# Kernel tuning notes

Hardware: AMD Instinct MI355X
Metric: run time of the kernel (lower is better)

## Reference

```python
import jax, jax.numpy as jnp
import numpy as np

B, T, S, E, H = 2, 2048, 2048, 1024, 16
DH = E // H

def setup_inputs() -> dict:
    key = jax.random.key(0)
    ks = jax.random.split(key, 12)
    sc = 1.0 / np.sqrt(E)
    inp = {
        'query': jax.random.normal(ks[0], (B, T, E), jnp.float32),
        'key':   jax.random.normal(ks[1], (B, S, E), jnp.float32),
        'value': jax.random.normal(ks[2], (B, S, E), jnp.float32),
        'Wq': jax.random.normal(ks[3], (E, E), jnp.float32) * sc,
        'bq': jnp.zeros((E,), jnp.float32),
        'Wk': jax.random.normal(ks[4], (E, E), jnp.float32) * sc,
        'bk': jnp.zeros((E,), jnp.float32),
        'Wv': jax.random.normal(ks[5], (E, E), jnp.float32) * sc,
        'bv': jnp.zeros((E,), jnp.float32),
        'Wo': jax.random.normal(ks[6], (E, E), jnp.float32) * sc,
        'bo': jnp.zeros((E,), jnp.float32),
    }
    return inp

def reference(query, key, value, Wq, bq, Wk, bk, Wv, bv, Wo, bo):
    # Linear projections (torch nn.Linear: x @ W.T + b)
    Q = query @ Wq.T + bq          # [B,T,E]
    K = key   @ Wk.T + bk          # [B,S,E]
    V = value @ Wv.T + bv          # [B,S,E]
    # split heads -> [B,H,L,DH]
    Q = Q.reshape(B, T, H, DH).transpose(0, 2, 1, 3)
    K = K.reshape(B, S, H, DH).transpose(0, 2, 1, 3)
    V = V.reshape(B, S, H, DH).transpose(0, 2, 1, 3)
    scores = jnp.einsum('bhtd,bhsd->bhts', Q, K) / jnp.sqrt(jnp.float32(DH))
    attn = jax.nn.softmax(scores, axis=-1)            # [B,H,T,S]
    out = jnp.einsum('bhts,bhsd->bhtd', attn, V)      # [B,H,T,DH]
    out = out.transpose(0, 2, 1, 3).reshape(B, T, E)
    out = out @ Wo.T + bo                             # [B,T,E]
    attn_avg = attn.mean(axis=1)                      # average_attn_weights=True
    return out, attn_avg
```

## Files before the change

kernel.cpp:

```cpp
#include <hip/hip_runtime.h>

#define DEV __device__ __forceinline__

typedef __attribute__((ext_vector_type(8))) short short8;
typedef __attribute__((ext_vector_type(4))) float floatx4;
typedef __attribute__((ext_vector_type(2))) unsigned int uint2v;
typedef unsigned short u16;

DEV u16 f2bf(float f) {
  unsigned int u = __float_as_uint(f);
  u += 0x7fffu + ((u >> 16) & 1u);
  return (u16)(u >> 16);
}

DEV unsigned int pk2bf(float a, float b) {
  unsigned int ua = __float_as_uint(a) + 0x8000u;
  unsigned int ub = __float_as_uint(b) + 0x8000u;
  return (ua >> 16) | (ub & 0xffff0000u);
}

DEV void load16_to_lds(const void* g, void* l) {
  __builtin_amdgcn_global_load_lds(
      (const __attribute__((address_space(1))) unsigned int*)g,
      (__attribute__((address_space(3))) unsigned int*)l, 16, 0, 0);
}

#define MFMA16(A, B, C) __builtin_amdgcn_mfma_f32_16x16x32_bf16(A, B, C, 0, 0, 0)
#define EXP2(x) __builtin_amdgcn_exp2f(x)

#define QSCALE 0.18033688011112042f

DEV void stage_block(const u16* src_row0, int k0, int ln, void* ldsbase) {
  int r = ln >> 2;
  int p = ((ln & 3) - (ln >> 4)) & 3;
  load16_to_lds((const char*)(src_row0 + (size_t)r * 1024 + k0) + p * 16, ldsbase);
}
DEV const short8* frag_addr(const u16* base, int blk, int c, int q) {
  int slot = c * 4 + ((q + (c >> 2)) & 3);
  return (const short8*)(base + blk * 512 + slot * 8);
}

__global__ __launch_bounds__(256) void cvt_all(
    const float* __restrict__ w0, const float* __restrict__ w1,
    const float* __restrict__ w2, const float* __restrict__ w3,
    const float* __restrict__ a0, const float* __restrict__ a1, const float* __restrict__ a2,
    u16* __restrict__ e0, u16* __restrict__ e1, u16* __restrict__ e2, u16* __restrict__ e3,
    u16* __restrict__ f0, u16* __restrict__ f1, u16* __restrict__ f2) {
  const int t = blockIdx.y;
  const float* s;
  u16* d;
  size_t base;
  if (t < 4) {
    s = t == 0 ? w0 : t == 1 ? w1 : t == 2 ? w2 : w3;
    d = t == 0 ? e0 : t == 1 ? e1 : t == 2 ? e2 : e3;
    base = 0;
  } else {
    int a = (t - 4) >> 2;
    s = a == 0 ? a0 : a == 1 ? a1 : a2;
    d = a == 0 ? f0 : a == 1 ? f1 : f2;
    base = (size_t)((t - 4) & 3) * 1048576;
  }
  size_t i = base + (size_t)(blockIdx.x * 256 + threadIdx.x) * 4;
  float4 v = *(const float4*)(s + i);
  ushort4 o;
  o.x = f2bf(v.x); o.y = f2bf(v.y); o.z = f2bf(v.z); o.w = f2bf(v.w);
  *(ushort4*)(d + i) = o;
}

__global__ __launch_bounds__(256) void qkv_gemm(
    const u16* __restrict__ qb, const u16* __restrict__ kb, const u16* __restrict__ vb,
    const u16* __restrict__ wq, const u16* __restrict__ wk, const u16* __restrict__ wv,
    const float* __restrict__ bq, const float* __restrict__ bk, const float* __restrict__ bv,
    u16* __restrict__ Qh, u16* __restrict__ Kh, u16* __restrict__ VT) {
  __shared__ __align__(16) u16 As[4096];
  __shared__ __align__(16) u16 Bs[4096];
  const int tid = threadIdx.x;
  const int w = tid >> 6, ln = tid & 63, q = ln >> 4, c = ln & 15;
  const int wr = w >> 1, wc = w & 1;
  const int z = blockIdx.z;
  const int m0 = (z == 2 ? blockIdx.x : blockIdx.y) * 128;
  const int n0 = (z == 2 ? blockIdx.y : blockIdx.x) * 128;
  const u16* Asrc = z == 0 ? qb : (z == 1 ? kb : wv);
  const u16* Bsrc = z == 0 ? wq : (z == 1 ? wk : vb);

  floatx4 acc[4][4];
#pragma unroll
  for (int i = 0; i < 4; ++i)
#pragma unroll
    for (int j = 0; j < 4; ++j) acc[i][j] = (floatx4){0.f, 0.f, 0.f, 0.f};

  for (int k0 = 0; k0 < 1024; k0 += 32) {
#pragma unroll
    for (int it = 0; it < 2; ++it) {
      int I = w * 2 + it;
      stage_block(Asrc + (size_t)(m0 + I * 16) * 1024, k0, ln, (char*)As + I * 1024);
      stage_block(Bsrc + (size_t)(n0 + I * 16) * 1024, k0, ln, (char*)Bs + I * 1024);
    }
    __syncthreads();
    short8 a[4], bb[4];
#pragma unroll
    for (int mt = 0; mt < 4; ++mt) a[mt] = *frag_addr(As, wr * 4 + mt, c, q);
#pragma unroll
    for (int nt = 0; nt < 4; ++nt) bb[nt] = *frag_addr(Bs, wc * 4 + nt, c, q);
#pragma unroll
    for (int mt = 0; mt < 4; ++mt)
#pragma unroll
      for (int nt = 0; nt < 4; ++nt) acc[mt][nt] = MFMA16(a[mt], bb[nt], acc[mt][nt]);
    __syncthreads();
  }

  if (z <= 1) {
    const float* bias = z ? bk : bq;
    u16* dst = z ? Kh : Qh;
    const float scale = z ? 1.0f : QSCALE;
    float bn[4];
#pragma unroll
    for (int nt = 0; nt < 4; ++nt) bn[nt] = bias[n0 + wc * 64 + nt * 16 + c];
#pragma unroll
    for (int mt = 0; mt < 4; ++mt)
#pragma unroll
      for (int r = 0; r < 4; ++r) {
        int m = m0 + wr * 64 + mt * 16 + 4 * q + r;
        int bbv = m >> 11, t = m & 2047;
#pragma unroll
        for (int nt = 0; nt < 4; ++nt) {
          int n = n0 + wc * 64 + nt * 16 + c;
          dst[((size_t)(bbv * 16 + (n >> 6)) * 2048 + t) * 64 + (n & 63)] =
              f2bf((acc[mt][nt][r] + bn[nt]) * scale);
        }
      }
  } else {
    float bm[4][4];
#pragma unroll
    for (int mt = 0; mt < 4; ++mt)
#pragma unroll
      for (int r = 0; r < 4; ++r) bm[mt][r] = bv[m0 + wr * 64 + mt * 16 + 4 * q + r];
#pragma unroll
    for (int mt = 0; mt < 4; ++mt)
#pragma unroll
      for (int r = 0; r < 4; ++r) {
        int d = m0 + wr * 64 + mt * 16 + 4 * q + r;
        int hh = d >> 6, dl = d & 63;
#pragma unroll
        for (int nt = 0; nt < 4; ++nt) {
          int s = n0 + wc * 64 + nt * 16 + c;
          int bbv = s >> 11, sl = s & 2047;
          VT[((size_t)(bbv * 16 + hh) * 64 + dl) * 2048 + sl] = f2bf(acc[mt][nt][r] + bm[mt][r]);
        }
      }
  }
}

__global__ __launch_bounds__(256) void oproj_gemm(const u16* __restrict__ Ap, const u16* __restrict__ Wp,
                                                  const float* __restrict__ bias, float* __restrict__ out) {
  __shared__ __align__(16) u16 As[4096];
  __shared__ __align__(16) u16 Bs[2048];
  const int tid = threadIdx.x;
  const int w = tid >> 6, ln = tid & 63, q = ln >> 4, c = ln & 15;
  const int wr = w >> 1, wc = w & 1;
  const int n0 = blockIdx.x * 64, m0 = blockIdx.y * 128;

  floatx4 acc[4][2];
#pragma unroll
  for (int i = 0; i < 4; ++i)
#pragma unroll
    for (int j = 0; j < 2; ++j) acc[i][j] = (floatx4){0.f, 0.f, 0.f, 0.f};

  for (int k0 = 0; k0 < 1024; k0 += 32) {
#pragma unroll
    for (int j = 0; j < 3; ++j) {
      int idx = w * 3 + j;
      if (idx < 8) {
        stage_block(Ap + (size_t)(m0 + idx * 16) * 1024, k0, ln, (char*)As + idx * 1024);
      } else {
        int bi = idx - 8;
        stage_block(Wp + (size_t)(n0 + bi * 16) * 1024, k0, ln, (char*)Bs + bi * 1024);
      }
    }
    __syncthreads();
    short8 a[4], bb[2];
#pragma unroll
    for (int mt = 0; mt < 4; ++mt) a[mt] = *frag_addr(As, wr * 4 + mt, c, q);
#pragma unroll
    for (int nt = 0; nt < 2; ++nt) bb[nt] = *frag_addr(Bs, wc * 2 + nt, c, q);
#pragma unroll
    for (int mt = 0; mt < 4; ++mt)
#pragma unroll
      for (int nt = 0; nt < 2; ++nt) acc[mt][nt] = MFMA16(a[mt], bb[nt], acc[mt][nt]);
    __syncthreads();
  }

  float bn[2];
#pragma unroll
  for (int nt = 0; nt < 2; ++nt) bn[nt] = bias[n0 + wc * 32 + nt * 16 + c];
#pragma unroll
  for (int mt = 0; mt < 4; ++mt)
#pragma unroll
    for (int r = 0; r < 4; ++r) {
      int m = m0 + wr * 64 + mt * 16 + 4 * q + r;
#pragma unroll
      for (int nt = 0; nt < 2; ++nt)
        out[(size_t)m * 1024 + n0 + wc * 32 + nt * 16 + c] = acc[mt][nt][r] + bn[nt];
    }
}

__global__ __launch_bounds__(256) void flash_attn(const u16* __restrict__ Qh, const u16* __restrict__ Kh,
                                                  const u16* __restrict__ VhT, u16* __restrict__ Obuf,
                                                  float* __restrict__ l_ws) {
  __shared__ __align__(16) u16 Ks[4096];
  __shared__ __align__(16) u16 VTs[4096];
  __shared__ __align__(16) u16 Ps[4][1152];
  const int tid = threadIdx.x;
  const int w = tid >> 6, ln = tid & 63, q = ln >> 4, c = ln & 15;
  const int t0 = blockIdx.x * 64, h = blockIdx.y, b = blockIdx.z;
  const size_t bh = (size_t)(b * 16 + h);
  const u16* Qbase = Qh + bh * 131072;
  const u16* Kbase = Kh + bh * 131072;
  const u16* Vbase = VhT + bh * 131072;

  short8 qf0, qf1;
  {
    const u16* qr = Qbase + (size_t)(t0 + w * 16 + c) * 64 + q * 8;
    qf0 = *(const short8*)qr;
    qf1 = *(const short8*)(qr + 32);
  }
  floatx4 oacc[4];
  float lacc = 0.f;
#pragma unroll
  for (int j = 0; j < 4; ++j) oacc[j] = (floatx4){0.f, 0.f, 0.f, 0.f};

  const int srow = ln >> 3;
  const int sch = (ln & 7) ^ srow;
  const int cx = c & 7;

  for (int s0 = 0; s0 < 2048; s0 += 64) {
#pragma unroll
    for (int it = 0; it < 2; ++it) {
      int I = w * 2 + it;
      int row = I * 8 + srow;
      load16_to_lds((const char*)Kbase + ((size_t)(s0 + row) * 64 + sch * 8) * 2, (char*)Ks + I * 1024);
      load16_to_lds((const char*)Vbase + ((size_t)row * 2048 + s0 + sch * 8) * 2, (char*)VTs + I * 1024);
    }
    __syncthreads();
#pragma unroll
    for (int st = 0; st < 4; ++st) {
      const int row = st * 16 + c;
      short8 k0 = *(const short8*)(Ks + row * 64 + ((q ^ cx) << 3));
      short8 k1 = *(const short8*)(Ks + row * 64 + (((4 + q) ^ cx) << 3));
      floatx4 zz = (floatx4){0.f, 0.f, 0.f, 0.f};
      zz = MFMA16(k0, qf0, zz);
      zz = MFMA16(k1, qf1, zz);
      float e0 = EXP2(zz[0]), e1 = EXP2(zz[1]), e2 = EXP2(zz[2]), e3 = EXP2(zz[3]);
      lacc += (e0 + e1) + (e2 + e3);
      uint2v pk = {pk2bf(e0, e1), pk2bf(e2, e3)};
      *(uint2v*)(&Ps[w][c * 72 + st * 16 + 4 * q]) = pk;
    }
    short8 pf0 = *(const short8*)(&Ps[w][c * 72 + q * 8]);
    short8 pf1 = *(const short8*)(&Ps[w][c * 72 + 32 + q * 8]);
#pragma unroll
    for (int dt = 0; dt < 4; ++dt) {
      const int row = dt * 16 + c;
      short8 v0 = *(const short8*)(VTs + row * 64 + ((q ^ cx) << 3));
      short8 v1 = *(const short8*)(VTs + row * 64 + (((4 + q) ^ cx) << 3));
      oacc[dt] = MFMA16(pf0, v0, oacc[dt]);
      oacc[dt] = MFMA16(pf1, v1, oacc[dt]);
    }
    __syncthreads();
  }
  {
    float v = lacc;
    v += __shfl_xor(v, 16);
    v += __shfl_xor(v, 32);
    lacc = v;
    if (q == 0) l_ws[bh * 2048 + t0 + w * 16 + c] = v;
  }
#pragma unroll
  for (int r = 0; r < 4; ++r) {
    float lv = __shfl(lacc, 4 * q + r);
    float inv = __builtin_amdgcn_rcpf(lv);
    const int t = t0 + w * 16 + 4 * q + r;
#pragma unroll
    for (int dt = 0; dt < 4; ++dt)
      Obuf[((size_t)b * 2048 + t) * 1024 + h * 64 + dt * 16 + c] = f2bf(oacc[dt][r] * inv);
  }
}

__global__ __launch_bounds__(256) void attn_avg_k(const u16* __restrict__ Qh, const u16* __restrict__ Kh,
                                                  const float* __restrict__ l_ws, float* __restrict__ out2) {
  __shared__ __align__(16) u16 Ks[2][4096];
  const int tid = threadIdx.x;
  const int w = tid >> 6, ln = tid & 63, q = ln >> 4, c = ln & 15;
  const int s0 = blockIdx.x * 64, t0 = blockIdx.y * 128, b = blockIdx.z;
  const int srow = ln >> 3;
  const int sch = (ln & 7) ^ srow;
  const int cx = c & 7;

  floatx4 acc[2][4];
#pragma unroll
  for (int i = 0; i < 2; ++i)
#pragma unroll
    for (int j = 0; j < 4; ++j) acc[i][j] = (floatx4){0.f, 0.f, 0.f, 0.f};

#pragma unroll
  for (int it = 0; it < 2; ++it) {
    int I = w * 2 + it;
    int row = I * 8 + srow;
    load16_to_lds((const char*)(Kh + (size_t)(b * 16) * 131072) + ((size_t)(s0 + row) * 64 + sch * 8) * 2,
                  (char*)Ks[0] + I * 1024);
  }

  for (int h = 0; h < 16; ++h) {
    const size_t bh = (size_t)(b * 16 + h);
    const u16* ks = Ks[h & 1];
    __syncthreads();
    if (h < 15) {
      const u16* Kn = Kh + (bh + 1) * 131072;
#pragma unroll
      for (int it = 0; it < 2; ++it) {
        int I = w * 2 + it;
        int row = I * 8 + srow;
        load16_to_lds((const char*)Kn + ((size_t)(s0 + row) * 64 + sch * 8) * 2,
                      (char*)Ks[(h + 1) & 1] + I * 1024);
      }
    }
    short8 qf[2][2];
    float linv[2];
#pragma unroll
    for (int blk = 0; blk < 2; ++blk) {
      const u16* qr = Qh + bh * 131072 + (size_t)(t0 + w * 32 + blk * 16 + c) * 64 + q * 8;
      qf[blk][0] = *(const short8*)qr;
      qf[blk][1] = *(const short8*)(qr + 32);
      linv[blk] = __builtin_amdgcn_rcpf(l_ws[bh * 2048 + t0 + w * 32 + blk * 16 + c]) * 0.0625f;
    }
#pragma unroll
    for (int st = 0; st < 4; ++st) {
      const int row = st * 16 + c;
      short8 k0 = *(const short8*)(ks + row * 64 + ((q ^ cx) << 3));
      short8 k1 = *(const short8*)(ks + row * 64 + (((4 + q) ^ cx) << 3));
#pragma unroll
      for (int blk = 0; blk < 2; ++blk) {
        floatx4 zz = (floatx4){0.f, 0.f, 0.f, 0.f};
        zz = MFMA16(k0, qf[blk][0], zz);
        zz = MFMA16(k1, qf[blk][1], zz);
#pragma unroll
        for (int r = 0; r < 4; ++r) acc[blk][st][r] += EXP2(zz[r]) * linv[blk];
      }
    }
  }
#pragma unroll
  for (int blk = 0; blk < 2; ++blk) {
    const size_t t = (size_t)t0 + w * 32 + blk * 16 + c;
#pragma unroll
    for (int st = 0; st < 4; ++st) {
      float4 o;
      o.x = acc[blk][st][0]; o.y = acc[blk][st][1]; o.z = acc[blk][st][2]; o.w = acc[blk][st][3];
      *(float4*)(out2 + ((size_t)b * 2048 + t) * 2048 + s0 + st * 16 + 4 * q) = o;
    }
  }
}

extern "C" void kernel_launch(void* const* d_in, const int* in_sizes, int n_in,
                              void* d_out, int out_size, void* d_ws, size_t ws_size,
                              hipStream_t stream) {
  const float* query = (const float*)d_in[0];
  const float* key = (const float*)d_in[1];
  const float* value = (const float*)d_in[2];
  const float* Wq = (const float*)d_in[3];
  const float* bq = (const float*)d_in[4];
  const float* Wk = (const float*)d_in[5];
  const float* bk = (const float*)d_in[6];
  const float* Wv = (const float*)d_in[7];
  const float* bv = (const float*)d_in[8];
  const float* Wo = (const float*)d_in[9];
  const float* bo = (const float*)d_in[10];

  char* ws = (char*)d_ws;
  const size_t MB = 1024 * 1024;
  u16* wWq = (u16*)(ws + 0 * MB);
  u16* wWk = (u16*)(ws + 2 * MB);
  u16* wWv = (u16*)(ws + 4 * MB);
  u16* wWo = (u16*)(ws + 6 * MB);
  u16* wQh = (u16*)(ws + 8 * MB);
  u16* wKh = (u16*)(ws + 16 * MB);
  u16* wVT = (u16*)(ws + 24 * MB);
  u16* wO = (u16*)(ws + 32 * MB);
  float* wl = (float*)(ws + 40 * MB);
  float* out = (float*)d_out;
  float* out2 = out + (size_t)4194304;

  u16* qb = (u16*)out2;
  u16* kb = qb + 4194304;
  u16* vb = kb + 4194304;

  cvt_all<<<dim3(1024, 16), 256, 0, stream>>>(Wq, Wk, Wv, Wo, query, key, value,
                                              wWq, wWk, wWv, wWo, qb, kb, vb);
  qkv_gemm<<<dim3(8, 32, 3), 256, 0, stream>>>(qb, kb, vb, wWq, wWk, wWv,
                                               bq, bk, bv, wQh, wKh, wVT);
  flash_attn<<<dim3(32, 16, 2), 256, 0, stream>>>(wQh, wKh, wVT, wO, wl);
  attn_avg_k<<<dim3(32, 16, 2), 256, 0, stream>>>(wQh, wKh, wl, out2);
  oproj_gemm<<<dim3(16, 32), 256, 0, stream>>>(wO, wWo, bo, out);
}
```

Before: 302.7 us.

## Double-buffer K/V tiles in flash attention with 512-thread blocks

The flash attention kernel now uses 512-thread blocks covering 128 query rows and double-buffered K/V LDS tiles. The next tile is prefetched while the current one is computed, which removes one barrier per iteration. It also replaces the manual bf16 packing with the hardware v_cvt_pk_bf16_f32 instruction and raises wave priority around the MFMA sections. The trade-off is more LDS per block and a different rounding mode for P (round-to-nearest-even instead of add-and-truncate), and each load is now issued once per wave instead of twice.

```diff
diff --git a/kernel.cpp b/kernel.cpp
--- a/kernel.cpp
+++ b/kernel.cpp
@@ -13,10 +13,10 @@
   return (u16)(u >> 16);
 }
 
-DEV unsigned int pk2bf(float a, float b) {
-  unsigned int ua = __float_as_uint(a) + 0x8000u;
-  unsigned int ub = __float_as_uint(b) + 0x8000u;
-  return (ua >> 16) | (ub & 0xffff0000u);
+DEV unsigned int cvtpk(float a, float b) {
+  unsigned int r;
+  asm("v_cvt_pk_bf16_f32 %0, %1, %2" : "=v"(r) : "v"(a), "v"(b));
+  return r;
 }
 
 DEV void load16_to_lds(const void* g, void* l) {
@@ -204,15 +204,15 @@
     }
 }
 
-__global__ __launch_bounds__(256) void flash_attn(const u16* __restrict__ Qh, const u16* __restrict__ Kh,
-                                                  const u16* __restrict__ VhT, u16* __restrict__ Obuf,
-                                                  float* __restrict__ l_ws) {
-  __shared__ __align__(16) u16 Ks[4096];
-  __shared__ __align__(16) u16 VTs[4096];
-  __shared__ __align__(16) u16 Ps[4][1152];
+__global__ __launch_bounds__(512, 4) void flash_attn(const u16* __restrict__ Qh, const u16* __restrict__ Kh,
+                                                     const u16* __restrict__ VhT, u16* __restrict__ Obuf,
+                                                     float* __restrict__ l_ws) {
+  __shared__ __align__(16) u16 Ks[2][4096];
+  __shared__ __align__(16) u16 VTs[2][4096];
+  __shared__ __align__(16) u16 Ps[8][1152];
   const int tid = threadIdx.x;
   const int w = tid >> 6, ln = tid & 63, q = ln >> 4, c = ln & 15;
-  const int t0 = blockIdx.x * 64, h = blockIdx.y, b = blockIdx.z;
+  const int t0 = blockIdx.x * 128, h = blockIdx.y, b = blockIdx.z;
   const size_t bh = (size_t)(b * 16 + h);
   const u16* Qbase = Qh + bh * 131072;
   const u16* Kbase = Kh + bh * 131072;
@@ -232,40 +232,51 @@
   const int srow = ln >> 3;
   const int sch = (ln & 7) ^ srow;
   const int cx = c & 7;
-
+  const int row = w * 8 + srow;
+
+  load16_to_lds((const char*)Kbase + ((size_t)row * 64 + sch * 8) * 2, (char*)Ks[0] + w * 1024);
+  load16_to_lds((const char*)Vbase + ((size_t)row * 2048 + sch * 8) * 2, (char*)VTs[0] + w * 1024);
+
+  int cur = 0;
   for (int s0 = 0; s0 < 2048; s0 += 64) {
-#pragma unroll
-    for (int it = 0; it < 2; ++it) {
-      int I = w * 2 + it;
-      int row = I * 8 + srow;
-      load16_to_lds((const char*)Kbase + ((size_t)(s0 + row) * 64 + sch * 8) * 2, (char*)Ks + I * 1024);
-      load16_to_lds((const char*)Vbase + ((size_t)row * 2048 + s0 + sch * 8) * 2, (char*)VTs + I * 1024);
-    }
-    __syncthreads();
+    __syncthreads();
+    if (s0 + 64 < 2048) {
+      const int nb = cur ^ 1;
+      load16_to_lds((const char*)Kbase + ((size_t)(s0 + 64 + row) * 64 + sch * 8) * 2,
+                    (char*)Ks[nb] + w * 1024);
+      load16_to_lds((const char*)Vbase + ((size_t)row * 2048 + (s0 + 64) + sch * 8) * 2,
+                    (char*)VTs[nb] + w * 1024);
+    }
+    const u16* ks = Ks[cur];
+    const u16* vs = VTs[cur];
 #pragma unroll
     for (int st = 0; st < 4; ++st) {
-      const int row = st * 16 + c;
-      short8 k0 = *(const short8*)(Ks + row * 64 + ((q ^ cx) << 3));
-      short8 k1 = *(const short8*)(Ks + row * 64 + (((4 + q) ^ cx) << 3));
+      const int rr = st * 16 + c;
+      short8 k0 = *(const short8*)(ks + rr * 64 + ((q ^ cx) << 3));
+      short8 k1 = *(const short8*)(ks + rr * 64 + (((4 + q) ^ cx) << 3));
       floatx4 zz = (floatx4){0.f, 0.f, 0.f, 0.f};
+      __builtin_amdgcn_s_setprio(1);
       zz = MFMA16(k0, qf0, zz);
       zz = MFMA16(k1, qf1, zz);
+      __builtin_amdgcn_s_setprio(0);
       float e0 = EXP2(zz[0]), e1 = EXP2(zz[1]), e2 = EXP2(zz[2]), e3 = EXP2(zz[3]);
       lacc += (e0 + e1) + (e2 + e3);
-      uint2v pk = {pk2bf(e0, e1), pk2bf(e2, e3)};
+      uint2v pk = {cvtpk(e0, e1), cvtpk(e2, e3)};
       *(uint2v*)(&Ps[w][c * 72 + st * 16 + 4 * q]) = pk;
     }
     short8 pf0 = *(const short8*)(&Ps[w][c * 72 + q * 8]);
     short8 pf1 = *(const short8*)(&Ps[w][c * 72 + 32 + q * 8]);
+    __builtin_amdgcn_s_setprio(1);
 #pragma unroll
     for (int dt = 0; dt < 4; ++dt) {
-      const int row = dt * 16 + c;
-      short8 v0 = *(const short8*)(VTs + row * 64 + ((q ^ cx) << 3));
-      short8 v1 = *(const short8*)(VTs + row * 64 + (((4 + q) ^ cx) << 3));
+      const int rr = dt * 16 + c;
+      short8 v0 = *(const short8*)(vs + rr * 64 + ((q ^ cx) << 3));
+      short8 v1 = *(const short8*)(vs + rr * 64 + (((4 + q) ^ cx) << 3));
       oacc[dt] = MFMA16(pf0, v0, oacc[dt]);
       oacc[dt] = MFMA16(pf1, v1, oacc[dt]);
     }
-    __syncthreads();
+    __builtin_amdgcn_s_setprio(0);
+    cur ^= 1;
   }
   {
     float v = lacc;
@@ -396,7 +407,7 @@
                                               wWq, wWk, wWv, wWo, qb, kb, vb);
   qkv_gemm<<<dim3(8, 32, 3), 256, 0, stream>>>(qb, kb, vb, wWq, wWk, wWv,
                                                bq, bk, bv, wQh, wKh, wVT);
-  flash_attn<<<dim3(32, 16, 2), 256, 0, stream>>>(wQh, wKh, wVT, wO, wl);
+  flash_attn<<<dim3(16, 16, 2), 512, 0, stream>>>(wQh, wKh, wVT, wO, wl);
   attn_avg_k<<<dim3(32, 16, 2), 256, 0, stream>>>(wQh, wKh, wl, out2);
   oproj_gemm<<<dim3(16, 32), 256, 0, stream>>>(wO, wWo, bo, out);
 }
```

Result: faster. 289.5 us (-4.4%).
